# Kernel optimization log

Measured on AMD Instinct MI355X. Metric: run time of the kernel, lower is better.

Reference implementation:

```python
import jax, jax.numpy as jnp
import numpy as np

NUM_EXPERTS = 8
AUX_LOSS_COEF = 0.01


def setup_inputs() -> dict:
    key = jax.random.key(0)
    ks = jax.random.split(key, 5)
    B, S, D, E, H = 4, 2048, 1024, NUM_EXPERTS, 4096
    scale = 0.02  # typical init scale so gelu/softmax stay in sane ranges
    return {
        "hidden_states": jax.random.normal(ks[0], (B, S, D), dtype=jnp.float32),
        "router_w": jax.random.normal(ks[1], (D, E), dtype=jnp.float32) * scale,
        "router_b": jnp.zeros((E,), dtype=jnp.float32),
        "w1": jax.random.normal(ks[2], (E, D, H), dtype=jnp.float32) * scale,
        "b1": jnp.zeros((E, H), dtype=jnp.float32),
        "w2": jax.random.normal(ks[3], (E, H, D), dtype=jnp.float32) * scale,
        "b2": jnp.zeros((E, D), dtype=jnp.float32),
    }


def reference(hidden_states, router_w, router_b, w1, b1, w2, b2):
    B, S, D = hidden_states.shape
    E = w1.shape[0]
    x = hidden_states.reshape(-1, D)  # [T, D] flattened tokens

    # Switch router: top-1 expert, combine weight = softmax prob of chosen expert
    logits = x @ router_w + router_b                      # [T, E]
    probs = jax.nn.softmax(logits, axis=-1)               # [T, E]
    sel = jnp.argmax(logits, axis=-1)                     # [T] int
    gate = jnp.take_along_axis(probs, sel[:, None], axis=1)[:, 0]  # [T]

    # Expert FFNs: per-expert Linear -> gelu -> Linear, masked top-1 combine.
    # Loop is over the small fixed expert count (structurally distinct weights).
    out = jnp.zeros_like(x)
    for e in range(E):
        h = jax.nn.gelu(x @ w1[e] + b1[e])                # [T, H]
        ye = h @ w2[e] + b2[e]                            # [T, D]
        mask = (sel == e).astype(x.dtype)
        out = out + (mask * gate)[:, None] * ye

    # Switch load-balancing auxiliary loss
    mean_probs = probs.mean(axis=0)                       # [E]
    assignments = jnp.mean(jax.nn.one_hot(sel, E, dtype=x.dtype), axis=0)  # [E]
    aux_loss = jnp.sum(mean_probs * assignments) * E
    total_loss = AUX_LOSS_COEF * aux_loss

    return out.reshape(B, S, D), total_loss
```

## Files before the change

kernel.cpp:

```cpp
#include <hip/hip_runtime.h>
#include <cstdint>

typedef __bf16 bf16_t;
typedef __attribute__((ext_vector_type(8))) __bf16 bf16x8;
typedef __attribute__((ext_vector_type(4))) float f32x4;
typedef unsigned short ushort_t;

#define TOKENS 8192
#define DIM 1024
#define HID 4096
#define NEXP 8


__device__ __forceinline__ void gl_lds16(const void* g, void* l) {
  __builtin_amdgcn_global_load_lds(
      (__attribute__((address_space(1))) void*)(void*)g,
      (__attribute__((address_space(3))) void*)l, 16, 0, 0);
}

__device__ __forceinline__ float gelu_fast(float x) {
  float x2 = x * x;
  float z2 = x * (1.59576912f + 0.07135482f * x2);
  float e = __expf(-z2);
  return x * __builtin_amdgcn_rcpf(1.f + e);
}

#define PW8() do { __builtin_amdgcn_sched_barrier(0);                      \
    asm volatile("s_waitcnt vmcnt(8)" ::: "memory");                       \
    __builtin_amdgcn_sched_barrier(0); __builtin_amdgcn_s_barrier();       \
    __builtin_amdgcn_sched_barrier(0); } while (0)
#define PW0() do { __builtin_amdgcn_sched_barrier(0);                      \
    asm volatile("s_waitcnt vmcnt(0)" ::: "memory");                       \
    __builtin_amdgcn_sched_barrier(0); __builtin_amdgcn_s_barrier();       \
    __builtin_amdgcn_sched_barrier(0); } while (0)
#define TB() do { __builtin_amdgcn_sched_barrier(0);                       \
    __builtin_amdgcn_s_barrier(); __builtin_amdgcn_sched_barrier(0); } while (0)

__global__ void router_kernel(const float* __restrict__ x, const float* __restrict__ rw,
                              const float* __restrict__ rbias, bf16_t* __restrict__ xb,
                              int* __restrict__ sel, float* __restrict__ gate,
                              float* __restrict__ pprob, int* __restrict__ pcnt) {
  __shared__ float sprob[NEXP];
  __shared__ int scnt[NEXP];
  int t = threadIdx.x, lane = t & 63, wave = t >> 6;
  if (t < NEXP) { sprob[t] = 0.f; scnt[t] = 0; }
  __syncthreads();
  int tok = blockIdx.x * 4 + wave;
  const float* xp = x + (size_t)tok * DIM + lane * 16;
  float acc[NEXP];
#pragma unroll
  for (int e = 0; e < NEXP; ++e) acc[e] = 0.f;
  ushort_t xv[16];
#pragma unroll
  for (int j = 0; j < 16; j += 4) {
    float4 v = *(const float4*)(xp + j);
    const float* wr = rw + (size_t)(lane * 16 + j) * NEXP;
    float c[4] = {v.x, v.y, v.z, v.w};
#pragma unroll
    for (int d = 0; d < 4; ++d) {
      xv[j + d] = __builtin_bit_cast(ushort_t, (bf16_t)c[d]);
#pragma unroll
      for (int e = 0; e < NEXP; ++e) acc[e] += c[d] * wr[d * NEXP + e];
    }
  }
  {
    uint4* xop = (uint4*)(xb + (size_t)tok * DIM + lane * 16);
    xop[0] = ((uint4*)xv)[0];
    xop[1] = ((uint4*)xv)[1];
  }
#pragma unroll
  for (int s = 1; s < 64; s <<= 1)
#pragma unroll
    for (int e = 0; e < NEXP; ++e) acc[e] += __shfl_xor(acc[e], s);
  if (lane == 0) {
    float lg[NEXP];
#pragma unroll
    for (int e = 0; e < NEXP; ++e) lg[e] = acc[e] + rbias[e];
    float mx = lg[0]; int am = 0;
#pragma unroll
    for (int e = 1; e < NEXP; ++e) if (lg[e] > mx) { mx = lg[e]; am = e; }
    float p[NEXP]; float se = 0.f;
#pragma unroll
    for (int e = 0; e < NEXP; ++e) { p[e] = __expf(lg[e] - mx); se += p[e]; }
    float inv = 1.f / se;
#pragma unroll
    for (int e = 0; e < NEXP; ++e) { p[e] *= inv; atomicAdd(&sprob[e], p[e]); }
    sel[tok] = am;
    gate[tok] = p[am];
    atomicAdd(&scnt[am], 1);
  }
  __syncthreads();
  if (t < NEXP) {
    pprob[blockIdx.x * NEXP + t] = sprob[t];
    pcnt[blockIdx.x * NEXP + t] = scnt[t];
  }
}

__global__ void tcvt2_kernel(const float* __restrict__ w1, const float* __restrict__ w2,
                             bf16_t* __restrict__ w1t, bf16_t* __restrict__ w2t) {
  __shared__ float tile[64][65];
  int y = blockIdx.y;
  int which = y >> 3, e = y & 7;
  int R = which ? HID : DIM;
  int C = which ? DIM : HID;
  const float* src = (which ? w2 : w1) + (size_t)e * R * C;
  bf16_t* dst = (which ? w2t : w1t) + (size_t)e * R * C;
  int cbt = C >> 6;
  int rt = blockIdx.x / cbt, ct = blockIdx.x % cbt;
  int rb = rt * 64, cb = ct * 64;
  int t = threadIdx.x;
  int r = t >> 2, cq = (t & 3) * 16;
  const float* sp = src + (size_t)(rb + r) * C + cb + cq;
#pragma unroll
  for (int j = 0; j < 16; j += 4) {
    float4 v = *(const float4*)(sp + j);
    tile[r][cq + j + 0] = v.x; tile[r][cq + j + 1] = v.y;
    tile[r][cq + j + 2] = v.z; tile[r][cq + j + 3] = v.w;
  }
  __syncthreads();
  int oc = t >> 2, orr = (t & 3) * 16;
  ushort_t tmp[16];
#pragma unroll
  for (int j = 0; j < 16; ++j) {
    bf16_t b = (bf16_t)tile[orr + j][oc];
    tmp[j] = __builtin_bit_cast(ushort_t, b);
  }
  uint4* dp = (uint4*)(dst + (size_t)(cb + oc) * R + rb + orr);
  dp[0] = ((uint4*)tmp)[0];
  dp[1] = ((uint4*)tmp)[1];
}

__global__ void reduce_kernel(const float* __restrict__ pprob, const int* __restrict__ pcnt,
                              int nb, int* __restrict__ meta, float* __restrict__ loss_out) {
  __shared__ float fred[256];
  __shared__ int ired[256];
  int t = threadIdx.x;
  int e = t & 7, i0 = t >> 3;
  float fs = 0.f; int is = 0;
  for (int i = i0; i < nb; i += 32) { fs += pprob[i * 8 + e]; is += pcnt[i * 8 + e]; }
  fred[t] = fs; ired[t] = is;
  __syncthreads();
  if (t < NEXP) {
    float tp = 0.f; int tc = 0;
    for (int j = 0; j < 32; ++j) { tp += fred[j * 8 + t]; tc += ired[j * 8 + t]; }
    meta[t] = tc;
    fred[t] = tp;
    meta[16 + t] = 0;
  }
  __syncthreads();
  if (t == 0) {
    int off = 0; float loss = 0.f; int s = 0;
    for (int q = 0; q < NEXP; ++q) {
      int c = meta[q];
      meta[8 + q] = off;
      int ntile = (c + 127) >> 7;
      for (int m = 0; m < ntile; ++m) meta[32 + s++] = (q << 16) | m;
      off += c;
      loss += (fred[q] / (float)TOKENS) * ((float)c / (float)TOKENS);
    }
    meta[24] = s;
    *loss_out = loss * (float)NEXP * 0.01f;
  }
}

__global__ void scatter_kernel(const int* __restrict__ sel, int* __restrict__ meta,
                               int* __restrict__ idxl) {
  int tok = blockIdx.x * 256 + threadIdx.x;
  int lane = threadIdx.x & 63;
  int e = sel[tok];
  const int* offsets = meta + 8;
  int* cursors = meta + 16;
#pragma unroll
  for (int ex = 0; ex < NEXP; ++ex) {
    unsigned long long mask = __ballot(e == ex);
    if (e == ex) {
      int leader = __ffsll(mask) - 1;
      int total = __popcll(mask);
      int rank = __popcll(mask & ((1ull << lane) - 1ull));
      int base = 0;
      if (lane == leader) base = atomicAdd(&cursors[ex], total);
      base = __shfl(base, leader);
      idxl[offsets[ex] + base + rank] = tok;
    }
  }
}

#define G_STG(Ab, Bb, KT) do {                                             \
    _Pragma("unroll")                                                      \
    for (int c_ = 0; c_ < 4; ++c_) {                                       \
      gl_lds16(ap[c_] + (KT) * 64, &Ab[(c_ * 4 + wave) * 512]);            \
      gl_lds16(bp[c_] + (KT) * 64, &Bb[(c_ * 4 + wave) * 512]);            \
    }                                                                      \
  } while (0)

#define G_CMP(Ab, Bb) do {                                                 \
    bf16x8 af[2][4], bv[2][4];                                             \
    _Pragma("unroll")                                                      \
    for (int kk = 0; kk < 2; ++kk) {                                       \
      _Pragma("unroll")                                                    \
      for (int m = 0; m < 4; ++m) {                                        \
        int row = wrow * 64 + m * 16 + l15;                                \
        af[kk][m] = *(const bf16x8*)&Ab[row * 64 + (((kk*4+g) ^ (l15 & 7)) * 8)]; \
      }                                                                    \
      _Pragma("unroll")                                                    \
      for (int n = 0; n < 4; ++n) {                                        \
        int row = wcol * 64 + n * 16 + l15;                                \
        bv[kk][n] = *(const bf16x8*)&Bb[row * 64 + (((kk*4+g) ^ (l15 & 7)) * 8)]; \
      }                                                                    \
    }                                                                      \
    _Pragma("unroll")                                                      \
    for (int kk = 0; kk < 2; ++kk)                                         \
      _Pragma("unroll")                                                    \
      for (int m = 0; m < 4; ++m)                                          \
        _Pragma("unroll")                                                  \
        for (int n = 0; n < 4; ++n)                                        \
          acc[m][n] = __builtin_amdgcn_mfma_f32_16x16x32_bf16(af[kk][m], bv[kk][n], acc[m][n], 0, 0, 0); \
  } while (0)

__global__ __launch_bounds__(256) void gemm1_kernel(
    const bf16_t* __restrict__ xb, const bf16_t* __restrict__ w1t,
    const float* __restrict__ b1, const int* __restrict__ idxl,
    const int* __restrict__ meta, bf16_t* __restrict__ h) {
  int slot = blockIdx.x;
  if (slot >= meta[24]) return;
  int tm = meta[32 + slot];
  int e = tm >> 16, mt = tm & 0xffff;
  int cnt = meta[e];
  int off = meta[8 + e];
  int mBase = mt * 128;
  int nBase = blockIdx.y * 128;
  __shared__ bf16_t A0[8192], A1[8192], B0[8192], B1[8192];
  int t = threadIdx.x, lane = t & 63, wave = t >> 6;
  int l15 = lane & 15, g = lane >> 4;
  int wrow = wave >> 1, wcol = wave & 1;
  f32x4 acc[4][4];
#pragma unroll
  for (int m = 0; m < 4; ++m)
#pragma unroll
    for (int n = 0; n < 4; ++n) acc[m][n] = (f32x4){0.f, 0.f, 0.f, 0.f};

  int lr = lane >> 3;
  int koff = (((lane & 7) ^ lr)) * 8;
  int c1 = cnt - 1;
  const bf16_t* ap[4];
  const bf16_t* bp[4];
  const bf16_t* wb = w1t + (size_t)e * HID * DIM;
#pragma unroll
  for (int c = 0; c < 4; ++c) {
    int r = 32 * c + 8 * wave + lr;
    int sl = mBase + r; sl = sl < c1 ? sl : c1;
    ap[c] = xb + (size_t)idxl[off + sl] * DIM + koff;
    bp[c] = wb + (size_t)(nBase + r) * DIM + koff;
  }

  G_STG(A0, B0, 0);
#pragma unroll 1
  for (int kt = 0; kt < DIM / 64 - 2; kt += 2) {
    G_STG(A1, B1, kt + 1); PW8(); G_CMP(A0, B0); TB();
    G_STG(A0, B0, kt + 2); PW8(); G_CMP(A1, B1); TB();
  }
  G_STG(A1, B1, DIM / 64 - 1); PW8(); G_CMP(A0, B0); TB();
  PW0(); G_CMP(A1, B1);

  float bias[4];
#pragma unroll
  for (int n = 0; n < 4; ++n) bias[n] = b1[e * HID + nBase + wcol * 64 + n * 16 + l15];
#pragma unroll
  for (int m = 0; m < 4; ++m) {
    int rb0 = mBase + wrow * 64 + m * 16 + g * 4;
#pragma unroll
    for (int j = 0; j < 4; ++j) {
      int r = rb0 + j;
      if (r < cnt) {
        bf16_t* hp = h + (size_t)(off + r) * HID + nBase + wcol * 64 + l15;
#pragma unroll
        for (int n = 0; n < 4; ++n)
          hp[n * 16] = (bf16_t)gelu_fast(acc[m][n][j] + bias[n]);
      }
    }
  }
}

__global__ __launch_bounds__(256) void gemm2_kernel(
    const bf16_t* __restrict__ h, const bf16_t* __restrict__ w2t,
    const float* __restrict__ b2, const int* __restrict__ idxl,
    const float* __restrict__ gate, const int* __restrict__ meta,
    float* __restrict__ out) {
  int slot = blockIdx.x;
  if (slot >= meta[24]) return;
  int tm = meta[32 + slot];
  int e = tm >> 16, mt = tm & 0xffff;
  int cnt = meta[e];
  int off = meta[8 + e];
  int mBase = mt * 128;
  int nBase = blockIdx.y * 128;
  __shared__ bf16_t A0[8192], A1[8192], B0[8192], B1[8192];
  int t = threadIdx.x, lane = t & 63, wave = t >> 6;
  int l15 = lane & 15, g = lane >> 4;
  int wrow = wave >> 1, wcol = wave & 1;
  f32x4 acc[4][4];
#pragma unroll
  for (int m = 0; m < 4; ++m)
#pragma unroll
    for (int n = 0; n < 4; ++n) acc[m][n] = (f32x4){0.f, 0.f, 0.f, 0.f};

  int lr = lane >> 3;
  int koff = (((lane & 7) ^ lr)) * 8;
  int c1 = cnt - 1;
  const bf16_t* ap[4];
  const bf16_t* bp[4];
  const bf16_t* wb = w2t + (size_t)e * DIM * HID;
#pragma unroll
  for (int c = 0; c < 4; ++c) {
    int r = 32 * c + 8 * wave + lr;
    int sl = mBase + r; sl = sl < c1 ? sl : c1;
    ap[c] = h + (size_t)(off + sl) * HID + koff;
    bp[c] = wb + (size_t)(nBase + r) * HID + koff;
  }

  G_STG(A0, B0, 0);
#pragma unroll 1
  for (int kt = 0; kt < HID / 64 - 2; kt += 2) {
    G_STG(A1, B1, kt + 1); PW8(); G_CMP(A0, B0); TB();
    G_STG(A0, B0, kt + 2); PW8(); G_CMP(A1, B1); TB();
  }
  G_STG(A1, B1, HID / 64 - 1); PW8(); G_CMP(A0, B0); TB();
  PW0(); G_CMP(A1, B1);

  float bias[4];
#pragma unroll
  for (int n = 0; n < 4; ++n) bias[n] = b2[e * DIM + nBase + wcol * 64 + n * 16 + l15];
#pragma unroll
  for (int m = 0; m < 4; ++m) {
    int rb0 = mBase + wrow * 64 + m * 16 + g * 4;
#pragma unroll
    for (int j = 0; j < 4; ++j) {
      int r = rb0 + j;
      if (r < cnt) {
        int tok = idxl[off + r];
        float gg = gate[tok];
        float* op = out + (size_t)tok * DIM + nBase + wcol * 64 + l15;
#pragma unroll
        for (int n = 0; n < 4; ++n)
          op[n * 16] = gg * (acc[m][n][j] + bias[n]);
      }
    }
  }
}

extern "C" void kernel_launch(void* const* d_in, const int* in_sizes, int n_in,
                              void* d_out, int out_size, void* d_ws, size_t ws_size,
                              hipStream_t stream) {
  const float* hs = (const float*)d_in[0];
  const float* rw = (const float*)d_in[1];
  const float* rb = (const float*)d_in[2];
  const float* w1 = (const float*)d_in[3];
  const float* b1 = (const float*)d_in[4];
  const float* w2 = (const float*)d_in[5];
  const float* b2 = (const float*)d_in[6];
  float* out = (float*)d_out;
  char* ws = (char*)d_ws;

  bf16_t* xb   = (bf16_t*)(ws + 0);
  bf16_t* w1t  = (bf16_t*)(ws + 16777216);
  bf16_t* w2t  = (bf16_t*)(ws + 83886080);
  bf16_t* hbuf = (bf16_t*)(ws + 150994944);
  int*   sel   = (int*)  (ws + 219152384);
  float* gate  = (float*)(ws + 219185152);
  int*   idxl  = (int*)  (ws + 219217920);
  float* pprob = (float*)(ws + 219250688);
  int*   pcnt  = (int*)  (ws + 219316224);
  int*   meta  = (int*)  (ws + 219381760);

  router_kernel<<<2048, 256, 0, stream>>>(hs, rw, rb, xb, sel, gate, pprob, pcnt);
  tcvt2_kernel<<<dim3(1024, 16), 256, 0, stream>>>(w1, w2, w1t, w2t);
  reduce_kernel<<<1, 256, 0, stream>>>(pprob, pcnt, 2048, meta, out + (out_size - 1));
  scatter_kernel<<<32, 256, 0, stream>>>(sel, meta, idxl);
  gemm1_kernel<<<dim3(72, 32), 256, 0, stream>>>(xb, w1t, b1, idxl, meta, hbuf);
  gemm2_kernel<<<dim3(72, 8), 256, 0, stream>>>(hbuf, w2t, b2, idxl, gate, meta, out);
}
```

Baseline: 427.1 us.

## Enlarge grouped-GEMM tiles to 512-thread blocks and add XCD-aware block remapping

gemm1 moves from 128x128 tiles with 256 threads to 256x256 tiles with 512 threads (8 waves, each holding 8x4 accumulators). gemm2 moves to 128x256 tiles with 512 threads. The router reduce step now emits separate tile schedules for the two GEMMs, and the flat block id is remapped so consecutive logical tiles land on the same XCD to improve L2 reuse. The goal is higher arithmetic intensity and less repeated weight and activation traffic. The costs are more register pressure from 128 accumulator floats in gemm1, larger LDS use (128KB in gemm1), and more padding waste on partial expert tiles.

```diff
diff --git a/kernel.cpp b/kernel.cpp
--- a/kernel.cpp
+++ b/kernel.cpp
@@ -25,16 +25,27 @@
   return x * __builtin_amdgcn_rcpf(1.f + e);
 }
 
-#define PW8() do { __builtin_amdgcn_sched_barrier(0);                      \
-    asm volatile("s_waitcnt vmcnt(8)" ::: "memory");                       \
-    __builtin_amdgcn_sched_barrier(0); __builtin_amdgcn_s_barrier();       \
-    __builtin_amdgcn_sched_barrier(0); } while (0)
-#define PW0() do { __builtin_amdgcn_sched_barrier(0);                      \
-    asm volatile("s_waitcnt vmcnt(0)" ::: "memory");                       \
-    __builtin_amdgcn_sched_barrier(0); __builtin_amdgcn_s_barrier();       \
-    __builtin_amdgcn_sched_barrier(0); } while (0)
-#define TB() do { __builtin_amdgcn_sched_barrier(0);                       \
-    __builtin_amdgcn_s_barrier(); __builtin_amdgcn_sched_barrier(0); } while (0)
+template <int N>
+__device__ __forceinline__ void pwait() {
+  __builtin_amdgcn_sched_barrier(0);
+  if constexpr (N == 8) asm volatile("s_waitcnt vmcnt(8)" ::: "memory");
+  else if constexpr (N == 6) asm volatile("s_waitcnt vmcnt(6)" ::: "memory");
+  else asm volatile("s_waitcnt vmcnt(0)" ::: "memory");
+  __builtin_amdgcn_sched_barrier(0);
+  __builtin_amdgcn_s_barrier();
+  __builtin_amdgcn_sched_barrier(0);
+}
+__device__ __forceinline__ void tbar() {
+  __builtin_amdgcn_sched_barrier(0);
+  __builtin_amdgcn_s_barrier();
+  __builtin_amdgcn_sched_barrier(0);
+}
+
+__device__ __forceinline__ int xcd_chunk(int f, int nwg) {
+  int q = nwg >> 3, r = nwg & 7;
+  int xcd = f & 7, pos = f >> 3;
+  return (xcd < r) ? (xcd * (q + 1) + pos) : (r * (q + 1) + (xcd - r) * q + pos);
+}
 
 __global__ void router_kernel(const float* __restrict__ x, const float* __restrict__ rw,
                               const float* __restrict__ rbias, bf16_t* __restrict__ xb,
@@ -149,16 +160,19 @@
   }
   __syncthreads();
   if (t == 0) {
-    int off = 0; float loss = 0.f; int s = 0;
+    int off = 0; float loss = 0.f; int s1 = 0, s2 = 0;
     for (int q = 0; q < NEXP; ++q) {
       int c = meta[q];
       meta[8 + q] = off;
-      int ntile = (c + 127) >> 7;
-      for (int m = 0; m < ntile; ++m) meta[32 + s++] = (q << 16) | m;
+      int nt1 = (c + 255) >> 8;
+      for (int m = 0; m < nt1; ++m) meta[32 + s1++] = (q << 16) | m;
+      int nt2 = (c + 127) >> 7;
+      for (int m = 0; m < nt2; ++m) meta[96 + s2++] = (q << 16) | m;
       off += c;
       loss += (fred[q] / (float)TOKENS) * ((float)c / (float)TOKENS);
     }
-    meta[24] = s;
+    meta[24] = s1;
+    meta[25] = s2;
     *loss_out = loss * (float)NEXP * 0.01f;
   }
 }
@@ -185,89 +199,86 @@
   }
 }
 
-#define G_STG(Ab, Bb, KT) do {                                             \
+#define STG1(Ab, Bb, KT) do {                                              \
     _Pragma("unroll")                                                      \
     for (int c_ = 0; c_ < 4; ++c_) {                                       \
-      gl_lds16(ap[c_] + (KT) * 64, &Ab[(c_ * 4 + wave) * 512]);            \
-      gl_lds16(bp[c_] + (KT) * 64, &Bb[(c_ * 4 + wave) * 512]);            \
+      gl_lds16(ap[c_] + (KT) * 64, Ab + c_ * 4096 + wave * 512);           \
+      gl_lds16(bp[c_] + (KT) * 64, Bb + c_ * 4096 + wave * 512);           \
     }                                                                      \
   } while (0)
 
-#define G_CMP(Ab, Bb) do {                                                 \
-    bf16x8 af[2][4], bv[2][4];                                             \
+#define CMP1(Ab, Bb) do {                                                  \
     _Pragma("unroll")                                                      \
     for (int kk = 0; kk < 2; ++kk) {                                       \
+      int ks = ((kk * 4 + g) ^ (l15 & 7)) * 8;                             \
+      bf16x8 bv[4];                                                        \
       _Pragma("unroll")                                                    \
-      for (int m = 0; m < 4; ++m) {                                        \
-        int row = wrow * 64 + m * 16 + l15;                                \
-        af[kk][m] = *(const bf16x8*)&Ab[row * 64 + (((kk*4+g) ^ (l15 & 7)) * 8)]; \
-      }                                                                    \
+      for (int n = 0; n < 4; ++n)                                          \
+        bv[n] = *(const bf16x8*)&Bb[(wcol * 64 + n * 16 + l15) * 64 + ks]; \
       _Pragma("unroll")                                                    \
-      for (int n = 0; n < 4; ++n) {                                        \
-        int row = wcol * 64 + n * 16 + l15;                                \
-        bv[kk][n] = *(const bf16x8*)&Bb[row * 64 + (((kk*4+g) ^ (l15 & 7)) * 8)]; \
+      for (int m = 0; m < 8; ++m) {                                        \
+        bf16x8 af = *(const bf16x8*)&Ab[(wrow * 128 + m * 16 + l15) * 64 + ks]; \
+        _Pragma("unroll")                                                  \
+        for (int n = 0; n < 4; ++n)                                        \
+          acc[m][n] = __builtin_amdgcn_mfma_f32_16x16x32_bf16(af, bv[n], acc[m][n], 0, 0, 0); \
       }                                                                    \
     }                                                                      \
-    _Pragma("unroll")                                                      \
-    for (int kk = 0; kk < 2; ++kk)                                         \
-      _Pragma("unroll")                                                    \
-      for (int m = 0; m < 4; ++m)                                          \
-        _Pragma("unroll")                                                  \
-        for (int n = 0; n < 4; ++n)                                        \
-          acc[m][n] = __builtin_amdgcn_mfma_f32_16x16x32_bf16(af[kk][m], bv[kk][n], acc[m][n], 0, 0, 0); \
   } while (0)
 
-__global__ __launch_bounds__(256) void gemm1_kernel(
+__global__ __launch_bounds__(512, 2) void gemm1_kernel(
     const bf16_t* __restrict__ xb, const bf16_t* __restrict__ w1t,
     const float* __restrict__ b1, const int* __restrict__ idxl,
     const int* __restrict__ meta, bf16_t* __restrict__ h) {
-  int slot = blockIdx.x;
+  int S = gridDim.x;
+  int f = blockIdx.y * S + blockIdx.x;
+  int lf = xcd_chunk(f, S * gridDim.y);
+  int slot = lf % S, nt = lf / S;
   if (slot >= meta[24]) return;
   int tm = meta[32 + slot];
   int e = tm >> 16, mt = tm & 0xffff;
   int cnt = meta[e];
   int off = meta[8 + e];
-  int mBase = mt * 128;
-  int nBase = blockIdx.y * 128;
-  __shared__ bf16_t A0[8192], A1[8192], B0[8192], B1[8192];
+  int mBase = mt * 256;
+  int nBase = nt * 256;
+  __shared__ bf16_t A0[16384], A1[16384], B0[16384], B1[16384];
   int t = threadIdx.x, lane = t & 63, wave = t >> 6;
   int l15 = lane & 15, g = lane >> 4;
-  int wrow = wave >> 1, wcol = wave & 1;
-  f32x4 acc[4][4];
-#pragma unroll
-  for (int m = 0; m < 4; ++m)
+  int wrow = wave >> 2, wcol = wave & 3;
+  f32x4 acc[8][4];
+#pragma unroll
+  for (int m = 0; m < 8; ++m)
 #pragma unroll
     for (int n = 0; n < 4; ++n) acc[m][n] = (f32x4){0.f, 0.f, 0.f, 0.f};
 
-  int lr = lane >> 3;
-  int koff = (((lane & 7) ^ lr)) * 8;
+  int lr3 = lane >> 3;
+  int koff = ((lane & 7) ^ lr3) * 8;
   int c1 = cnt - 1;
   const bf16_t* ap[4];
   const bf16_t* bp[4];
   const bf16_t* wb = w1t + (size_t)e * HID * DIM;
 #pragma unroll
   for (int c = 0; c < 4; ++c) {
-    int r = 32 * c + 8 * wave + lr;
+    int r = c * 64 + wave * 8 + lr3;
     int sl = mBase + r; sl = sl < c1 ? sl : c1;
     ap[c] = xb + (size_t)idxl[off + sl] * DIM + koff;
     bp[c] = wb + (size_t)(nBase + r) * DIM + koff;
   }
 
-  G_STG(A0, B0, 0);
+  STG1(A0, B0, 0);
 #pragma unroll 1
   for (int kt = 0; kt < DIM / 64 - 2; kt += 2) {
-    G_STG(A1, B1, kt + 1); PW8(); G_CMP(A0, B0); TB();
-    G_STG(A0, B0, kt + 2); PW8(); G_CMP(A1, B1); TB();
-  }
-  G_STG(A1, B1, DIM / 64 - 1); PW8(); G_CMP(A0, B0); TB();
-  PW0(); G_CMP(A1, B1);
+    STG1(A1, B1, kt + 1); pwait<8>(); CMP1(A0, B0); tbar();
+    STG1(A0, B0, kt + 2); pwait<8>(); CMP1(A1, B1); tbar();
+  }
+  STG1(A1, B1, DIM / 64 - 1); pwait<8>(); CMP1(A0, B0); tbar();
+  pwait<0>(); CMP1(A1, B1);
 
   float bias[4];
 #pragma unroll
   for (int n = 0; n < 4; ++n) bias[n] = b1[e * HID + nBase + wcol * 64 + n * 16 + l15];
 #pragma unroll
-  for (int m = 0; m < 4; ++m) {
-    int rb0 = mBase + wrow * 64 + m * 16 + g * 4;
+  for (int m = 0; m < 8; ++m) {
+    int rb0 = mBase + wrow * 128 + m * 16 + g * 4;
 #pragma unroll
     for (int j = 0; j < 4; ++j) {
       int r = rb0 + j;
@@ -281,51 +292,85 @@
   }
 }
 
-__global__ __launch_bounds__(256) void gemm2_kernel(
+#define STG2(Ab, Bb, KT) do {                                              \
+    _Pragma("unroll")                                                      \
+    for (int c_ = 0; c_ < 2; ++c_)                                         \
+      gl_lds16(ap[c_] + (KT) * 64, Ab + c_ * 4096 + wave * 512);           \
+    _Pragma("unroll")                                                      \
+    for (int c_ = 0; c_ < 4; ++c_)                                         \
+      gl_lds16(bp[c_] + (KT) * 64, Bb + c_ * 4096 + wave * 512);           \
+  } while (0)
+
+#define CMP2(Ab, Bb) do {                                                  \
+    _Pragma("unroll")                                                      \
+    for (int kk = 0; kk < 2; ++kk) {                                       \
+      int ks = ((kk * 4 + g) ^ (l15 & 7)) * 8;                             \
+      bf16x8 bv[4];                                                        \
+      _Pragma("unroll")                                                    \
+      for (int n = 0; n < 4; ++n)                                          \
+        bv[n] = *(const bf16x8*)&Bb[(wcol * 64 + n * 16 + l15) * 64 + ks]; \
+      _Pragma("unroll")                                                    \
+      for (int m = 0; m < 4; ++m) {                                        \
+        bf16x8 af = *(const bf16x8*)&Ab[(wrow * 64 + m * 16 + l15) * 64 + ks]; \
+        _Pragma("unroll")                                                  \
+        for (int n = 0; n < 4; ++n)                                        \
+          acc[m][n] = __builtin_amdgcn_mfma_f32_16x16x32_bf16(af, bv[n], acc[m][n], 0, 0, 0); \
+      }                                                                    \
+    }                                                                      \
+  } while (0)
+
+__global__ __launch_bounds__(512, 2) void gemm2_kernel(
     const bf16_t* __restrict__ h, const bf16_t* __restrict__ w2t,
     const float* __restrict__ b2, const int* __restrict__ idxl,
     const float* __restrict__ gate, const int* __restrict__ meta,
     float* __restrict__ out) {
-  int slot = blockIdx.x;
-  if (slot >= meta[24]) return;
-  int tm = meta[32 + slot];
+  int S = gridDim.x;
+  int f = blockIdx.y * S + blockIdx.x;
+  int lf = xcd_chunk(f, S * gridDim.y);
+  int slot = lf % S, nt = lf / S;
+  if (slot >= meta[25]) return;
+  int tm = meta[96 + slot];
   int e = tm >> 16, mt = tm & 0xffff;
   int cnt = meta[e];
   int off = meta[8 + e];
   int mBase = mt * 128;
-  int nBase = blockIdx.y * 128;
-  __shared__ bf16_t A0[8192], A1[8192], B0[8192], B1[8192];
+  int nBase = nt * 256;
+  __shared__ bf16_t A0[8192], A1[8192], B0[16384], B1[16384];
   int t = threadIdx.x, lane = t & 63, wave = t >> 6;
   int l15 = lane & 15, g = lane >> 4;
-  int wrow = wave >> 1, wcol = wave & 1;
+  int wrow = wave >> 2, wcol = wave & 3;
   f32x4 acc[4][4];
 #pragma unroll
   for (int m = 0; m < 4; ++m)
 #pragma unroll
     for (int n = 0; n < 4; ++n) acc[m][n] = (f32x4){0.f, 0.f, 0.f, 0.f};
 
-  int lr = lane >> 3;
-  int koff = (((lane & 7) ^ lr)) * 8;
+  int lr3 = lane >> 3;
+  int koff = ((lane & 7) ^ lr3) * 8;
   int c1 = cnt - 1;
-  const bf16_t* ap[4];
+  const bf16_t* ap[2];
   const bf16_t* bp[4];
   const bf16_t* wb = w2t + (size_t)e * DIM * HID;
 #pragma unroll
-  for (int c = 0; c < 4; ++c) {
-    int r = 32 * c + 8 * wave + lr;
+  for (int c = 0; c < 2; ++c) {
+    int r = c * 64 + wave * 8 + lr3;
     int sl = mBase + r; sl = sl < c1 ? sl : c1;
     ap[c] = h + (size_t)(off + sl) * HID + koff;
+  }
+#pragma unroll
+  for (int c = 0; c < 4; ++c) {
+    int r = c * 64 + wave * 8 + lr3;
     bp[c] = wb + (size_t)(nBase + r) * HID + koff;
   }
 
-  G_STG(A0, B0, 0);
+  STG2(A0, B0, 0);
 #pragma unroll 1
   for (int kt = 0; kt < HID / 64 - 2; kt += 2) {
-    G_STG(A1, B1, kt + 1); PW8(); G_CMP(A0, B0); TB();
-    G_STG(A0, B0, kt + 2); PW8(); G_CMP(A1, B1); TB();
-  }
-  G_STG(A1, B1, HID / 64 - 1); PW8(); G_CMP(A0, B0); TB();
-  PW0(); G_CMP(A1, B1);
+    STG2(A1, B1, kt + 1); pwait<6>(); CMP2(A0, B0); tbar();
+    STG2(A0, B0, kt + 2); pwait<6>(); CMP2(A1, B1); tbar();
+  }
+  STG2(A1, B1, HID / 64 - 1); pwait<6>(); CMP2(A0, B0); tbar();
+  pwait<0>(); CMP2(A1, B1);
 
   float bias[4];
 #pragma unroll
@@ -376,6 +421,6 @@
   tcvt2_kernel<<<dim3(1024, 16), 256, 0, stream>>>(w1, w2, w1t, w2t);
   reduce_kernel<<<1, 256, 0, stream>>>(pprob, pcnt, 2048, meta, out + (out_size - 1));
   scatter_kernel<<<32, 256, 0, stream>>>(sel, meta, idxl);
-  gemm1_kernel<<<dim3(72, 32), 256, 0, stream>>>(xb, w1t, b1, idxl, meta, hbuf);
-  gemm2_kernel<<<dim3(72, 8), 256, 0, stream>>>(hbuf, w2t, b2, idxl, gate, meta, out);
-}
+  gemm1_kernel<<<dim3(40, 16), 512, 0, stream>>>(xb, w1t, b1, idxl, meta, hbuf);
+  gemm2_kernel<<<dim3(72, 4), 512, 0, stream>>>(hbuf, w2t, b2, idxl, gate, meta, out);
+}
```

Result: slower. 440.5 us (+3.1%).
